# Kernel tuning notes

Hardware: AMD Instinct MI355X
Metric: run time of the kernel (lower is better)

Reference implementation:

```python
import jax, jax.numpy as jnp
import numpy as np

H = 128
G = 8192            # num session graphs
TOTAL = 409600      # total nodes across all graphs
MAX_ITEM = 10000


def setup_inputs() -> dict:
    key = jax.random.key(0)
    ks = jax.random.split(key, 16)
    rng = np.random.default_rng(0)
    # variable-length sections that sum exactly to TOTAL
    secs = rng.integers(10, 90, size=G - 1)
    last = TOTAL - int(secs.sum())
    assert last >= 1
    sections = np.concatenate([secs, [last]]).astype(np.int32)
    segment_ids = np.repeat(np.arange(G, dtype=np.int32), sections)
    last_idx = (np.cumsum(sections) - 1).astype(np.int32)

    s = 0.02
    inp = {
        "node_embedding": jax.random.normal(ks[0], (TOTAL, H), jnp.float32),
        "num_count": jax.random.uniform(ks[1], (TOTAL,), jnp.float32),
        "sections": jnp.asarray(sections),
        "segment_ids": jnp.asarray(segment_ids),
        "last_idx": jnp.asarray(last_idx),
        "item_embedding_table": jax.random.normal(ks[2], (MAX_ITEM, H), jnp.float32),
        "user_embedding": jax.random.normal(ks[3], (G, H), jnp.float32),
        "u_n_repeat": jnp.zeros((G, H), jnp.float32),
        "max_item_id": MAX_ITEM,
        "W1_w": jax.random.normal(ks[4], (H, H), jnp.float32) * s,
        "W1_b": jnp.zeros((H,), jnp.float32),
        "W2_w": jax.random.normal(ks[5], (H, H), jnp.float32) * s,
        "W2_b": jnp.zeros((H,), jnp.float32),
        "q_w": jax.random.normal(ks[6], (1, H), jnp.float32) * s,
        "q_b": jnp.zeros((1,), jnp.float32),
        "W3_w": jax.random.normal(ks[7], (H, 2 * H), jnp.float32) * s,
        "W3_b": jnp.zeros((H,), jnp.float32),
    }
    return inp


def reference(node_embedding, num_count, sections, segment_ids, last_idx,
              item_embedding_table, user_embedding, u_n_repeat, max_item_id,
              W1_w, W1_b, W2_w, W2_b, q_w, q_b, W3_w, W3_b):
    num_graphs = last_idx.shape[0]
    # last node of each graph, [G, H]
    v_n = node_embedding[last_idx]
    # broadcast last node back to every node of its graph (replaces torch.split repeat loop)
    v_n_rep = v_n[segment_ids]                          # [N, H]
    gate = jax.nn.sigmoid(v_n_rep @ W1_w.T + W1_b + node_embedding @ W2_w.T + W2_b)
    alpha = gate @ q_w.T + q_b                          # [N, 1]
    s_g_whole = num_count[:, None] * alpha * node_embedding  # [N, H]
    s_g = jax.ops.segment_sum(s_g_whole, segment_ids, num_segments=num_graphs)  # [G, H]
    s_h = jnp.concatenate([v_n, s_g], axis=1) @ W3_w.T + W3_b  # [G, H]
    return s_h
```

## Files before the change

### kernel.cpp

```cpp
#include <hip/hip_runtime.h>
#include <hip/hip_bf16.h>

#define H_DIM  128
#define NGRAPH 8192
#define NTOTAL 409600

typedef __attribute__((ext_vector_type(8))) short    s16x8;
typedef __attribute__((ext_vector_type(4))) float    f32x4;
typedef __attribute__((ext_vector_type(4))) unsigned u32x4;

__device__ __forceinline__ unsigned short f2bf(float f) {
    unsigned int u = __float_as_uint(f);
    unsigned int r = u + 0x7fffu + ((u >> 16) & 1u);
    return (unsigned short)(r >> 16);
}

__global__ void k0_w2(const float* __restrict__ W2w, unsigned short* __restrict__ w2bf) {
    int i = blockIdx.x * 256 + threadIdx.x;
    w2bf[i] = f2bf(W2w[i]);
}

__global__ __launch_bounds__(128) void k1_ag(
    const float* __restrict__ node_emb,
    const int*   __restrict__ last_idx,
    const float* __restrict__ W1w,
    const float* __restrict__ W1b,
    const float* __restrict__ W2b,
    float* __restrict__ a_g,
    float* __restrict__ s_g)
{
    __shared__ float vn[4][H_DIM];
    const int tid = threadIdx.x;
    const int g0  = blockIdx.x * 4;
    #pragma unroll
    for (int g = 0; g < 4; g++) {
        int li = last_idx[g0 + g];
        vn[g][tid] = node_emb[(size_t)li * H_DIM + tid];
        s_g[(size_t)(g0 + g) * H_DIM + tid] = 0.f;
    }
    __syncthreads();
    float b = W1b[tid] + W2b[tid];
    float a0 = b, a1 = b, a2 = b, a3 = b;
    const float* wrow = W1w + (size_t)tid * H_DIM;
    #pragma unroll 8
    for (int k = 0; k < H_DIM; k += 4) {
        float4 w = *reinterpret_cast<const float4*>(wrow + k);
        a0 += w.x * vn[0][k] + w.y * vn[0][k+1] + w.z * vn[0][k+2] + w.w * vn[0][k+3];
        a1 += w.x * vn[1][k] + w.y * vn[1][k+1] + w.z * vn[1][k+2] + w.w * vn[1][k+3];
        a2 += w.x * vn[2][k] + w.y * vn[2][k+1] + w.z * vn[2][k+2] + w.w * vn[2][k+3];
        a3 += w.x * vn[3][k] + w.y * vn[3][k+1] + w.z * vn[3][k+2] + w.w * vn[3][k+3];
    }
    a_g[(size_t)(g0 + 0) * H_DIM + tid] = a0;
    a_g[(size_t)(g0 + 1) * H_DIM + tid] = a1;
    a_g[(size_t)(g0 + 2) * H_DIM + tid] = a2;
    a_g[(size_t)(g0 + 3) * H_DIM + tid] = a3;
}

__global__ __launch_bounds__(256, 4) void k2_fused(
    const float* __restrict__ node_emb,
    const float* __restrict__ num_count,
    const int*   __restrict__ seg_ids,
    const float* __restrict__ a_g,
    const unsigned short* __restrict__ w2bf,
    const float* __restrict__ q_w,
    const float* __restrict__ q_b,
    float* __restrict__ s_g)
{
    __shared__ __align__(16) char w2s[H_DIM * 256];

    const int tid = threadIdx.x;
    {
        const uint4* wsrc = reinterpret_cast<const uint4*>(w2bf);
        #pragma unroll
        for (int i = 0; i < 8; i++) {
            int c = i * 256 + tid;
            uint4 v = wsrc[c];
            int byte = c << 4;
            int row  = byte >> 8;
            *reinterpret_cast<uint4*>(w2s + (byte ^ ((row & 7) << 4))) = v;
        }
    }

    const int lane = tid & 63;
    const int wid  = tid >> 6;
    const int l16 = lane & 15, lq = lane >> 4;
    const int nb  = (blockIdx.x * 4 + wid) * 16;

    const int   sgl = seg_ids[nb + l16];
    const float ncl = num_count[nb + l16];
    const float qb0 = q_b[0];

    s16x8 af[4];
    const float* nrow = node_emb + (size_t)(nb + l16) * H_DIM + lq * 8;
    #pragma unroll
    for (int ks = 0; ks < 4; ks++) {
        float4 f0 = *reinterpret_cast<const float4*>(nrow + ks * 32);
        float4 f1 = *reinterpret_cast<const float4*>(nrow + ks * 32 + 4);
        unsigned p0, p1, p2, p3;
        asm("v_cvt_pk_bf16_f32 %0, %1, %2" : "=v"(p0) : "v"(f0.x), "v"(f0.y));
        asm("v_cvt_pk_bf16_f32 %0, %1, %2" : "=v"(p1) : "v"(f0.z), "v"(f0.w));
        asm("v_cvt_pk_bf16_f32 %0, %1, %2" : "=v"(p2) : "v"(f1.x), "v"(f1.y));
        asm("v_cvt_pk_bf16_f32 %0, %1, %2" : "=v"(p3) : "v"(f1.z), "v"(f1.w));
        union { u32x4 u; s16x8 s; } cv;
        cv.u = u32x4{p0, p1, p2, p3};
        af[ks] = cv.s;
    }

    __syncthreads();

    f32x4 acc[8];
    #pragma unroll
    for (int nt = 0; nt < 8; nt++) acc[nt] = f32x4{0.f, 0.f, 0.f, 0.f};
    #pragma unroll
    for (int ks = 0; ks < 4; ks++) {
        #pragma unroll
        for (int nt = 0; nt < 8; nt++) {
            int row  = nt * 16 + l16;
            int byte = (row << 8) | ((lq * 8 + ks * 32) << 1);
            byte ^= (row & 7) << 4;
            s16x8 wfr = *reinterpret_cast<const s16x8*>(w2s + byte);
            acc[nt] = __builtin_amdgcn_mfma_f32_16x16x32_bf16(wfr, af[ks], acc[nt], 0, 0, 0);
        }
    }
    __builtin_amdgcn_sched_barrier(0);

    const float* agrow = a_g + (size_t)sgl * H_DIM + lq * 4;
    float p = 0.f;
    #pragma unroll
    for (int nt = 0; nt < 8; nt++) {
        float4 q4 = *reinterpret_cast<const float4*>(q_w + nt * 16 + lq * 4);
        float4 a4 = *reinterpret_cast<const float4*>(agrow + nt * 16);
        float zq[4] = {a4.x, a4.y, a4.z, a4.w};
        float qq[4] = {q4.x, q4.y, q4.z, q4.w};
        #pragma unroll
        for (int rr = 0; rr < 4; rr++) {
            float z = acc[nt][rr] + zq[rr];
            float e = __expf(-z);
            p += qq[rr] * __builtin_amdgcn_rcpf(1.f + e);
        }
    }
    p += __shfl_xor(p, 16, 64);
    p += __shfl_xor(p, 32, 64);
    const float coefl = ncl * (p + qb0);

    s16x8 ib[2];
    #pragma unroll
    for (int b = 0; b < 2; b++) {
        int kk = l16 + 16 * b;
        #pragma unroll
        for (int e = 0; e < 8; e++)
            ib[b][e] = (kk == lq * 8 + e) ? (short)0x3F80 : (short)0;
    }
    f32x4 accT[4][2];
    #pragma unroll
    for (int ks = 0; ks < 4; ks++)
        #pragma unroll
        for (int b = 0; b < 2; b++)
            accT[ks][b] = __builtin_amdgcn_mfma_f32_16x16x32_bf16(
                              af[ks], ib[b], f32x4{0.f, 0.f, 0.f, 0.f}, 0, 0, 0);

    int r0 = 0;
    while (r0 < 16) {
        const int cur = __shfl(sgl, r0, 64);
        unsigned long long diff = __ballot(sgl != cur) & 0xFFFFull;
        diff &= ~((1ull << r0) - 1ull);
        const int r1 = diff ? (int)__builtin_ctzll(diff) : 16;

        const float cmask = (sgl == cur) ? coefl : 0.f;
        float cm[4];
        #pragma unroll
        for (int rr = 0; rr < 4; rr++)
            cm[rr] = __shfl(cmask, lq * 4 + rr, 64);

        #pragma unroll
        for (int ks = 0; ks < 4; ks++) {
            #pragma unroll
            for (int b = 0; b < 2; b++) {
                float s = cm[0] * accT[ks][b][0] + cm[1] * accT[ks][b][1]
                        + cm[2] * accT[ks][b][2] + cm[3] * accT[ks][b][3];
                s += __shfl_xor(s, 16, 64);
                s += __shfl_xor(s, 32, 64);
                if (lq == 0)
                    atomicAdd(s_g + (size_t)cur * H_DIM + ks * 32 + b * 16 + l16, s);
            }
        }
        r0 = r1;
    }
}

__global__ __launch_bounds__(128) void k3_out(
    const float* __restrict__ node_emb,
    const int*   __restrict__ last_idx,
    const float* __restrict__ s_g,
    const float* __restrict__ W3w,
    const float* __restrict__ W3b,
    float* __restrict__ out)
{
    __shared__ float cat[8][2 * H_DIM];
    const int tid = threadIdx.x;
    const int g0  = blockIdx.x * 8;
    #pragma unroll
    for (int g = 0; g < 8; g++) {
        cat[g][tid]         = node_emb[(size_t)last_idx[g0 + g] * H_DIM + tid];
        cat[g][H_DIM + tid] = s_g[(size_t)(g0 + g) * H_DIM + tid];
    }
    __syncthreads();
    float acc[8];
    float b = W3b[tid];
    #pragma unroll
    for (int g = 0; g < 8; g++) acc[g] = b;
    const float* wrow = W3w + (size_t)tid * (2 * H_DIM);
    for (int k = 0; k < 2 * H_DIM; k += 4) {
        float4 w = *reinterpret_cast<const float4*>(wrow + k);
        #pragma unroll
        for (int g = 0; g < 8; g++)
            acc[g] += w.x * cat[g][k] + w.y * cat[g][k+1]
                    + w.z * cat[g][k+2] + w.w * cat[g][k+3];
    }
    #pragma unroll
    for (int g = 0; g < 8; g++)
        out[(size_t)(g0 + g) * H_DIM + tid] = acc[g];
}

extern "C" void kernel_launch(void* const* d_in, const int* in_sizes, int n_in,
                              void* d_out, int out_size, void* d_ws, size_t ws_size,
                              hipStream_t stream) {
    const float* node_emb  = (const float*)d_in[0];
    const float* num_count = (const float*)d_in[1];
    const int*   seg_ids   = (const int*)d_in[3];
    const int*   last_idx  = (const int*)d_in[4];
    const float* W1w = (const float*)d_in[9];
    const float* W1b = (const float*)d_in[10];
    const float* W2w = (const float*)d_in[11];
    const float* W2b = (const float*)d_in[12];
    const float* qw  = (const float*)d_in[13];
    const float* qb  = (const float*)d_in[14];
    const float* W3w = (const float*)d_in[15];
    const float* W3b = (const float*)d_in[16];
    float* out = (float*)d_out;

    char* ws = (char*)d_ws;
    float* a_g = (float*)(ws);
    float* s_g = (float*)(ws + (4u << 20));
    unsigned short* w2bf = (unsigned short*)(ws + (8u << 20));

    k0_w2   <<<64,          256, 0, stream>>>(W2w, w2bf);
    k1_ag   <<<NGRAPH / 4,  128, 0, stream>>>(node_emb, last_idx, W1w, W1b, W2b, a_g, s_g);
    k2_fused<<<NTOTAL / 64, 256, 0, stream>>>(node_emb, num_count, seg_ids, a_g,
                                              w2bf, qw, qb, s_g);
    k3_out  <<<NGRAPH / 8,  128, 0, stream>>>(node_emb, last_idx, s_g, W3w, W3b, out);
}
```

Before: 109.1 us.

## Make k2 waves loop over four node tiles with register prefetch

Each wave in the fused gate/segment-sum kernel now handles four 16-node tiles in a loop instead of one. The next tile's node rows, segment ids and counts are loaded into registers while the current tile is computed. The W2 LDS staging cost is spread over four times as many nodes, and the gate GEMM is split into two halves to limit accumulator registers. The grid shrinks by four and the occupancy hint drops from 4 to 3 blocks per CU, so there is less parallelism to hide latency.

```diff
diff --git a/kernel.cpp b/kernel.cpp
--- a/kernel.cpp
+++ b/kernel.cpp
@@ -56,7 +56,7 @@
     a_g[(size_t)(g0 + 3) * H_DIM + tid] = a3;
 }
 
-__global__ __launch_bounds__(256, 4) void k2_fused(
+__global__ __launch_bounds__(256, 3) void k2_fused(
     const float* __restrict__ node_emb,
     const float* __restrict__ num_count,
     const int*   __restrict__ seg_ids,
@@ -84,64 +84,8 @@
     const int lane = tid & 63;
     const int wid  = tid >> 6;
     const int l16 = lane & 15, lq = lane >> 4;
-    const int nb  = (blockIdx.x * 4 + wid) * 16;
-
-    const int   sgl = seg_ids[nb + l16];
-    const float ncl = num_count[nb + l16];
+    const int nbw = (blockIdx.x * 4 + wid) * 64;
     const float qb0 = q_b[0];
-
-    s16x8 af[4];
-    const float* nrow = node_emb + (size_t)(nb + l16) * H_DIM + lq * 8;
-    #pragma unroll
-    for (int ks = 0; ks < 4; ks++) {
-        float4 f0 = *reinterpret_cast<const float4*>(nrow + ks * 32);
-        float4 f1 = *reinterpret_cast<const float4*>(nrow + ks * 32 + 4);
-        unsigned p0, p1, p2, p3;
-        asm("v_cvt_pk_bf16_f32 %0, %1, %2" : "=v"(p0) : "v"(f0.x), "v"(f0.y));
-        asm("v_cvt_pk_bf16_f32 %0, %1, %2" : "=v"(p1) : "v"(f0.z), "v"(f0.w));
-        asm("v_cvt_pk_bf16_f32 %0, %1, %2" : "=v"(p2) : "v"(f1.x), "v"(f1.y));
-        asm("v_cvt_pk_bf16_f32 %0, %1, %2" : "=v"(p3) : "v"(f1.z), "v"(f1.w));
-        union { u32x4 u; s16x8 s; } cv;
-        cv.u = u32x4{p0, p1, p2, p3};
-        af[ks] = cv.s;
-    }
-
-    __syncthreads();
-
-    f32x4 acc[8];
-    #pragma unroll
-    for (int nt = 0; nt < 8; nt++) acc[nt] = f32x4{0.f, 0.f, 0.f, 0.f};
-    #pragma unroll
-    for (int ks = 0; ks < 4; ks++) {
-        #pragma unroll
-        for (int nt = 0; nt < 8; nt++) {
-            int row  = nt * 16 + l16;
-            int byte = (row << 8) | ((lq * 8 + ks * 32) << 1);
-            byte ^= (row & 7) << 4;
-            s16x8 wfr = *reinterpret_cast<const s16x8*>(w2s + byte);
-            acc[nt] = __builtin_amdgcn_mfma_f32_16x16x32_bf16(wfr, af[ks], acc[nt], 0, 0, 0);
-        }
-    }
-    __builtin_amdgcn_sched_barrier(0);
-
-    const float* agrow = a_g + (size_t)sgl * H_DIM + lq * 4;
-    float p = 0.f;
-    #pragma unroll
-    for (int nt = 0; nt < 8; nt++) {
-        float4 q4 = *reinterpret_cast<const float4*>(q_w + nt * 16 + lq * 4);
-        float4 a4 = *reinterpret_cast<const float4*>(agrow + nt * 16);
-        float zq[4] = {a4.x, a4.y, a4.z, a4.w};
-        float qq[4] = {q4.x, q4.y, q4.z, q4.w};
-        #pragma unroll
-        for (int rr = 0; rr < 4; rr++) {
-            float z = acc[nt][rr] + zq[rr];
-            float e = __expf(-z);
-            p += qq[rr] * __builtin_amdgcn_rcpf(1.f + e);
-        }
-    }
-    p += __shfl_xor(p, 16, 64);
-    p += __shfl_xor(p, 32, 64);
-    const float coefl = ncl * (p + qb0);
 
     s16x8 ib[2];
     #pragma unroll
@@ -151,40 +95,153 @@
         for (int e = 0; e < 8; e++)
             ib[b][e] = (kk == lq * 8 + e) ? (short)0x3F80 : (short)0;
     }
-    f32x4 accT[4][2];
-    #pragma unroll
-    for (int ks = 0; ks < 4; ks++)
-        #pragma unroll
-        for (int b = 0; b < 2; b++)
-            accT[ks][b] = __builtin_amdgcn_mfma_f32_16x16x32_bf16(
-                              af[ks], ib[b], f32x4{0.f, 0.f, 0.f, 0.f}, 0, 0, 0);
-
-    int r0 = 0;
-    while (r0 < 16) {
-        const int cur = __shfl(sgl, r0, 64);
-        unsigned long long diff = __ballot(sgl != cur) & 0xFFFFull;
-        diff &= ~((1ull << r0) - 1ull);
-        const int r1 = diff ? (int)__builtin_ctzll(diff) : 16;
-
-        const float cmask = (sgl == cur) ? coefl : 0.f;
-        float cm[4];
-        #pragma unroll
-        for (int rr = 0; rr < 4; rr++)
-            cm[rr] = __shfl(cmask, lq * 4 + rr, 64);
-
+
+    float4 rA[8];
+    int   sgN;
+    float ncN;
+    {
+        const float* nrow = node_emb + (size_t)(nbw + l16) * H_DIM + lq * 8;
         #pragma unroll
         for (int ks = 0; ks < 4; ks++) {
-            #pragma unroll
-            for (int b = 0; b < 2; b++) {
-                float s = cm[0] * accT[ks][b][0] + cm[1] * accT[ks][b][1]
-                        + cm[2] * accT[ks][b][2] + cm[3] * accT[ks][b][3];
-                s += __shfl_xor(s, 16, 64);
-                s += __shfl_xor(s, 32, 64);
-                if (lq == 0)
-                    atomicAdd(s_g + (size_t)cur * H_DIM + ks * 32 + b * 16 + l16, s);
-            }
-        }
-        r0 = r1;
+            rA[2 * ks]     = *reinterpret_cast<const float4*>(nrow + ks * 32);
+            rA[2 * ks + 1] = *reinterpret_cast<const float4*>(nrow + ks * 32 + 4);
+        }
+        sgN = seg_ids[nbw + l16];
+        ncN = num_count[nbw + l16];
+    }
+
+    __syncthreads();
+
+    #pragma unroll 1
+    for (int t = 0; t < 4; t++) {
+        const int   nb  = nbw + t * 16;
+        const int   sgl = sgN;
+        const float ncl = ncN;
+
+        s16x8 af[4];
+        #pragma unroll
+        for (int ks = 0; ks < 4; ks++) {
+            unsigned p0, p1, p2, p3;
+            asm("v_cvt_pk_bf16_f32 %0, %1, %2" : "=v"(p0) : "v"(rA[2*ks].x),   "v"(rA[2*ks].y));
+            asm("v_cvt_pk_bf16_f32 %0, %1, %2" : "=v"(p1) : "v"(rA[2*ks].z),   "v"(rA[2*ks].w));
+            asm("v_cvt_pk_bf16_f32 %0, %1, %2" : "=v"(p2) : "v"(rA[2*ks+1].x), "v"(rA[2*ks+1].y));
+            asm("v_cvt_pk_bf16_f32 %0, %1, %2" : "=v"(p3) : "v"(rA[2*ks+1].z), "v"(rA[2*ks+1].w));
+            union { u32x4 u; s16x8 s; } cv;
+            cv.u = u32x4{p0, p1, p2, p3};
+            af[ks] = cv.s;
+        }
+
+        if (t < 3) {
+            const float* nrow = node_emb + (size_t)(nb + 16 + l16) * H_DIM + lq * 8;
+            #pragma unroll
+            for (int ks = 0; ks < 4; ks++) {
+                rA[2 * ks]     = *reinterpret_cast<const float4*>(nrow + ks * 32);
+                rA[2 * ks + 1] = *reinterpret_cast<const float4*>(nrow + ks * 32 + 4);
+            }
+            sgN = seg_ids[nb + 16 + l16];
+            ncN = num_count[nb + 16 + l16];
+        }
+        __builtin_amdgcn_sched_barrier(0);
+
+        float p = 0.f;
+        const float* agrow = a_g + (size_t)sgl * H_DIM + lq * 4;
+        {
+            f32x4 accA[4];
+            #pragma unroll
+            for (int nt = 0; nt < 4; nt++) accA[nt] = f32x4{0.f, 0.f, 0.f, 0.f};
+            #pragma unroll
+            for (int ks = 0; ks < 4; ks++) {
+                #pragma unroll
+                for (int nt = 0; nt < 4; nt++) {
+                    int row  = nt * 16 + l16;
+                    int byte = (row << 8) | ((lq * 8 + ks * 32) << 1);
+                    byte ^= (row & 7) << 4;
+                    s16x8 wfr = *reinterpret_cast<const s16x8*>(w2s + byte);
+                    accA[nt] = __builtin_amdgcn_mfma_f32_16x16x32_bf16(wfr, af[ks], accA[nt], 0, 0, 0);
+                }
+            }
+            #pragma unroll
+            for (int nt = 0; nt < 4; nt++) {
+                float4 q4 = *reinterpret_cast<const float4*>(q_w + nt * 16 + lq * 4);
+                float4 a4 = *reinterpret_cast<const float4*>(agrow + nt * 16);
+                float zq[4] = {a4.x, a4.y, a4.z, a4.w};
+                float qq[4] = {q4.x, q4.y, q4.z, q4.w};
+                #pragma unroll
+                for (int rr = 0; rr < 4; rr++) {
+                    float z = accA[nt][rr] + zq[rr];
+                    float e = __expf(-z);
+                    p += qq[rr] * __builtin_amdgcn_rcpf(1.f + e);
+                }
+            }
+        }
+        {
+            f32x4 accB[4];
+            #pragma unroll
+            for (int nt = 0; nt < 4; nt++) accB[nt] = f32x4{0.f, 0.f, 0.f, 0.f};
+            #pragma unroll
+            for (int ks = 0; ks < 4; ks++) {
+                #pragma unroll
+                for (int nt = 0; nt < 4; nt++) {
+                    int row  = (nt + 4) * 16 + l16;
+                    int byte = (row << 8) | ((lq * 8 + ks * 32) << 1);
+                    byte ^= (row & 7) << 4;
+                    s16x8 wfr = *reinterpret_cast<const s16x8*>(w2s + byte);
+                    accB[nt] = __builtin_amdgcn_mfma_f32_16x16x32_bf16(wfr, af[ks], accB[nt], 0, 0, 0);
+                }
+            }
+            #pragma unroll
+            for (int nt = 0; nt < 4; nt++) {
+                float4 q4 = *reinterpret_cast<const float4*>(q_w + (nt + 4) * 16 + lq * 4);
+                float4 a4 = *reinterpret_cast<const float4*>(agrow + (nt + 4) * 16);
+                float zq[4] = {a4.x, a4.y, a4.z, a4.w};
+                float qq[4] = {q4.x, q4.y, q4.z, q4.w};
+                #pragma unroll
+                for (int rr = 0; rr < 4; rr++) {
+                    float z = accB[nt][rr] + zq[rr];
+                    float e = __expf(-z);
+                    p += qq[rr] * __builtin_amdgcn_rcpf(1.f + e);
+                }
+            }
+        }
+        p += __shfl_xor(p, 16, 64);
+        p += __shfl_xor(p, 32, 64);
+        const float coefl = ncl * (p + qb0);
+
+        f32x4 accT[4][2];
+        #pragma unroll
+        for (int ks = 0; ks < 4; ks++)
+            #pragma unroll
+            for (int b = 0; b < 2; b++)
+                accT[ks][b] = __builtin_amdgcn_mfma_f32_16x16x32_bf16(
+                                  af[ks], ib[b], f32x4{0.f, 0.f, 0.f, 0.f}, 0, 0, 0);
+
+        int r0 = 0;
+        while (r0 < 16) {
+            const int cur = __shfl(sgl, r0, 64);
+            unsigned long long diff = __ballot(sgl != cur) & 0xFFFFull;
+            diff &= ~((1ull << r0) - 1ull);
+            const int r1 = diff ? (int)__builtin_ctzll(diff) : 16;
+
+            const float cmask = (sgl == cur) ? coefl : 0.f;
+            float cm[4];
+            #pragma unroll
+            for (int rr = 0; rr < 4; rr++)
+                cm[rr] = __shfl(cmask, lq * 4 + rr, 64);
+
+            #pragma unroll
+            for (int ks = 0; ks < 4; ks++) {
+                #pragma unroll
+                for (int b = 0; b < 2; b++) {
+                    float s = cm[0] * accT[ks][b][0] + cm[1] * accT[ks][b][1]
+                            + cm[2] * accT[ks][b][2] + cm[3] * accT[ks][b][3];
+                    s += __shfl_xor(s, 16, 64);
+                    s += __shfl_xor(s, 32, 64);
+                    if (lq == 0)
+                        atomicAdd(s_g + (size_t)cur * H_DIM + ks * 32 + b * 16 + l16, s);
+                }
+            }
+            r0 = r1;
+        }
     }
 }
 
@@ -244,9 +301,9 @@
     float* s_g = (float*)(ws + (4u << 20));
     unsigned short* w2bf = (unsigned short*)(ws + (8u << 20));
 
-    k0_w2   <<<64,          256, 0, stream>>>(W2w, w2bf);
-    k1_ag   <<<NGRAPH / 4,  128, 0, stream>>>(node_emb, last_idx, W1w, W1b, W2b, a_g, s_g);
-    k2_fused<<<NTOTAL / 64, 256, 0, stream>>>(node_emb, num_count, seg_ids, a_g,
-                                              w2bf, qw, qb, s_g);
-    k3_out  <<<NGRAPH / 8,  128, 0, stream>>>(node_emb, last_idx, s_g, W3w, W3b, out);
-}
+    k0_w2   <<<64,           256, 0, stream>>>(W2w, w2bf);
+    k1_ag   <<<NGRAPH / 4,   128, 0, stream>>>(node_emb, last_idx, W1w, W1b, W2b, a_g, s_g);
+    k2_fused<<<NTOTAL / 256, 256, 0, stream>>>(node_emb, num_count, seg_ids, a_g,
+                                               w2bf, qw, qb, s_g);
+    k3_out  <<<NGRAPH / 8,   128, 0, stream>>>(node_emb, last_idx, s_g, W3w, W3b, out);
+}
```

Result: no change. 109.8 us (+0.6%).

## Assign one wave per graph segment and accumulate segment sums in registers

Applied to the files above, without the earlier changes.

The fused gate/segment-sum kernel now maps each wavefront to one whole graph, walking its nodes in 16-row chunks and accumulating the segment sum in registers. A single direct store per output row replaces the per-chunk atomicAdds. The oversized last graph is split across extra tail waves that still use atomics. This removes the per-chunk segment-boundary ballot loops and most global atomics, but adds load imbalance from variable graph lengths and wasted lanes on partial chunks.

```diff
diff --git a/kernel.cpp b/kernel.cpp
--- a/kernel.cpp
+++ b/kernel.cpp
@@ -4,6 +4,7 @@
 #define H_DIM  128
 #define NGRAPH 8192
 #define NTOTAL 409600
+#define TAILW  512
 
 typedef __attribute__((ext_vector_type(8))) short    s16x8;
 typedef __attribute__((ext_vector_type(4))) float    f32x4;
@@ -59,7 +60,7 @@
 __global__ __launch_bounds__(256, 4) void k2_fused(
     const float* __restrict__ node_emb,
     const float* __restrict__ num_count,
-    const int*   __restrict__ seg_ids,
+    const int*   __restrict__ last_idx,
     const float* __restrict__ a_g,
     const unsigned short* __restrict__ w2bf,
     const float* __restrict__ q_w,
@@ -82,66 +83,27 @@
     }
 
     const int lane = tid & 63;
-    const int wid  = tid >> 6;
     const int l16 = lane & 15, lq = lane >> 4;
-    const int nb  = (blockIdx.x * 4 + wid) * 16;
-
-    const int   sgl = seg_ids[nb + l16];
-    const float ncl = num_count[nb + l16];
-    const float qb0 = q_b[0];
-
-    s16x8 af[4];
-    const float* nrow = node_emb + (size_t)(nb + l16) * H_DIM + lq * 8;
-    #pragma unroll
-    for (int ks = 0; ks < 4; ks++) {
-        float4 f0 = *reinterpret_cast<const float4*>(nrow + ks * 32);
-        float4 f1 = *reinterpret_cast<const float4*>(nrow + ks * 32 + 4);
-        unsigned p0, p1, p2, p3;
-        asm("v_cvt_pk_bf16_f32 %0, %1, %2" : "=v"(p0) : "v"(f0.x), "v"(f0.y));
-        asm("v_cvt_pk_bf16_f32 %0, %1, %2" : "=v"(p1) : "v"(f0.z), "v"(f0.w));
-        asm("v_cvt_pk_bf16_f32 %0, %1, %2" : "=v"(p2) : "v"(f1.x), "v"(f1.y));
-        asm("v_cvt_pk_bf16_f32 %0, %1, %2" : "=v"(p3) : "v"(f1.z), "v"(f1.w));
-        union { u32x4 u; s16x8 s; } cv;
-        cv.u = u32x4{p0, p1, p2, p3};
-        af[ks] = cv.s;
-    }
-
-    __syncthreads();
-
-    f32x4 acc[8];
-    #pragma unroll
-    for (int nt = 0; nt < 8; nt++) acc[nt] = f32x4{0.f, 0.f, 0.f, 0.f};
-    #pragma unroll
-    for (int ks = 0; ks < 4; ks++) {
-        #pragma unroll
-        for (int nt = 0; nt < 8; nt++) {
-            int row  = nt * 16 + l16;
-            int byte = (row << 8) | ((lq * 8 + ks * 32) << 1);
-            byte ^= (row & 7) << 4;
-            s16x8 wfr = *reinterpret_cast<const s16x8*>(w2s + byte);
-            acc[nt] = __builtin_amdgcn_mfma_f32_16x16x32_bf16(wfr, af[ks], acc[nt], 0, 0, 0);
-        }
-    }
-    __builtin_amdgcn_sched_barrier(0);
-
-    const float* agrow = a_g + (size_t)sgl * H_DIM + lq * 4;
-    float p = 0.f;
-    #pragma unroll
-    for (int nt = 0; nt < 8; nt++) {
-        float4 q4 = *reinterpret_cast<const float4*>(q_w + nt * 16 + lq * 4);
-        float4 a4 = *reinterpret_cast<const float4*>(agrow + nt * 16);
-        float zq[4] = {a4.x, a4.y, a4.z, a4.w};
-        float qq[4] = {q4.x, q4.y, q4.z, q4.w};
-        #pragma unroll
-        for (int rr = 0; rr < 4; rr++) {
-            float z = acc[nt][rr] + zq[rr];
-            float e = __expf(-z);
-            p += qq[rr] * __builtin_amdgcn_rcpf(1.f + e);
-        }
-    }
-    p += __shfl_xor(p, 16, 64);
-    p += __shfl_xor(p, 32, 64);
-    const float coefl = ncl * (p + qb0);
+    const int item = __builtin_amdgcn_readfirstlane(blockIdx.x * 4 + (tid >> 6));
+
+    int g = 0, nstart = 0, nend = -1;
+    bool tail = false, valid = true;
+    if (item < NGRAPH - 1) {
+        g      = item;
+        nstart = item ? (last_idx[item - 1] + 1) : 0;
+        nend   = last_idx[item];
+    } else if (item < NGRAPH - 1 + TAILW) {
+        g    = NGRAPH - 1;
+        tail = true;
+        int base = last_idx[NGRAPH - 2] + 1;
+        int t0   = item - (NGRAPH - 1);
+        nstart   = base + t0 * 16;
+        int ge   = last_idx[NGRAPH - 1];
+        if (nstart > ge) valid = false;
+        else nend = min(ge, nstart + 15);
+    } else {
+        valid = false;
+    }
 
     s16x8 ib[2];
     #pragma unroll
@@ -151,40 +113,112 @@
         for (int e = 0; e < 8; e++)
             ib[b][e] = (kk == lq * 8 + e) ? (short)0x3F80 : (short)0;
     }
-    f32x4 accT[4][2];
-    #pragma unroll
-    for (int ks = 0; ks < 4; ks++)
-        #pragma unroll
-        for (int b = 0; b < 2; b++)
-            accT[ks][b] = __builtin_amdgcn_mfma_f32_16x16x32_bf16(
-                              af[ks], ib[b], f32x4{0.f, 0.f, 0.f, 0.f}, 0, 0, 0);
-
-    int r0 = 0;
-    while (r0 < 16) {
-        const int cur = __shfl(sgl, r0, 64);
-        unsigned long long diff = __ballot(sgl != cur) & 0xFFFFull;
-        diff &= ~((1ull << r0) - 1ull);
-        const int r1 = diff ? (int)__builtin_ctzll(diff) : 16;
-
-        const float cmask = (sgl == cur) ? coefl : 0.f;
-        float cm[4];
-        #pragma unroll
-        for (int rr = 0; rr < 4; rr++)
-            cm[rr] = __shfl(cmask, lq * 4 + rr, 64);
-
+
+    __syncthreads();
+    if (!valid) return;
+
+    const float qb0 = q_b[0];
+    const float* agrow = a_g + (size_t)g * H_DIM;
+
+    float sgacc[4][2] = {{0.f, 0.f}, {0.f, 0.f}, {0.f, 0.f}, {0.f, 0.f}};
+
+    for (int nb = nstart; nb <= nend; nb += 16) {
+        const int vcnt = nend - nb + 1;
+        const int idx  = min(nb + l16, nend);
+
+        const float* nrow = node_emb + (size_t)idx * H_DIM + lq * 8;
+        float4 f[8];
+        #pragma unroll
+        for (int ks = 0; ks < 4; ks++) {
+            f[2 * ks]     = *reinterpret_cast<const float4*>(nrow + ks * 32);
+            f[2 * ks + 1] = *reinterpret_cast<const float4*>(nrow + ks * 32 + 4);
+        }
+        const float ncl = num_count[idx];
+
+        s16x8 af[4];
+        #pragma unroll
+        for (int ks = 0; ks < 4; ks++) {
+            unsigned p0, p1, p2, p3;
+            asm("v_cvt_pk_bf16_f32 %0, %1, %2" : "=v"(p0) : "v"(f[2*ks].x),   "v"(f[2*ks].y));
+            asm("v_cvt_pk_bf16_f32 %0, %1, %2" : "=v"(p1) : "v"(f[2*ks].z),   "v"(f[2*ks].w));
+            asm("v_cvt_pk_bf16_f32 %0, %1, %2" : "=v"(p2) : "v"(f[2*ks+1].x), "v"(f[2*ks+1].y));
+            asm("v_cvt_pk_bf16_f32 %0, %1, %2" : "=v"(p3) : "v"(f[2*ks+1].z), "v"(f[2*ks+1].w));
+            union { u32x4 u; s16x8 s; } cv;
+            cv.u = u32x4{p0, p1, p2, p3};
+            af[ks] = cv.s;
+        }
+
+        f32x4 accT[4][2];
+        #pragma unroll
+        for (int ks = 0; ks < 4; ks++)
+            #pragma unroll
+            for (int b = 0; b < 2; b++)
+                accT[ks][b] = __builtin_amdgcn_mfma_f32_16x16x32_bf16(
+                                  af[ks], ib[b], f32x4{0.f, 0.f, 0.f, 0.f}, 0, 0, 0);
+
+        f32x4 acc[8];
+        #pragma unroll
+        for (int nt = 0; nt < 8; nt++) acc[nt] = f32x4{0.f, 0.f, 0.f, 0.f};
         #pragma unroll
         for (int ks = 0; ks < 4; ks++) {
             #pragma unroll
-            for (int b = 0; b < 2; b++) {
-                float s = cm[0] * accT[ks][b][0] + cm[1] * accT[ks][b][1]
-                        + cm[2] * accT[ks][b][2] + cm[3] * accT[ks][b][3];
-                s += __shfl_xor(s, 16, 64);
-                s += __shfl_xor(s, 32, 64);
-                if (lq == 0)
-                    atomicAdd(s_g + (size_t)cur * H_DIM + ks * 32 + b * 16 + l16, s);
+            for (int nt = 0; nt < 8; nt++) {
+                int row  = nt * 16 + l16;
+                int byte = (row << 8) | ((lq * 8 + ks * 32) << 1);
+                byte ^= (row & 7) << 4;
+                s16x8 wfr = *reinterpret_cast<const s16x8*>(w2s + byte);
+                acc[nt] = __builtin_amdgcn_mfma_f32_16x16x32_bf16(wfr, af[ks], acc[nt], 0, 0, 0);
             }
         }
-        r0 = r1;
+
+        float pp0 = 0.f, pp1 = 0.f, pp2 = 0.f, pp3 = 0.f;
+        #pragma unroll
+        for (int nt = 0; nt < 8; nt++) {
+            float4 q4 = *reinterpret_cast<const float4*>(q_w + nt * 16 + lq * 4);
+            float4 a4 = *reinterpret_cast<const float4*>(agrow + nt * 16 + lq * 4);
+            float z0 = acc[nt][0] + a4.x;
+            float z1 = acc[nt][1] + a4.y;
+            float z2 = acc[nt][2] + a4.z;
+            float z3 = acc[nt][3] + a4.w;
+            pp0 += q4.x * __builtin_amdgcn_rcpf(1.f + __expf(-z0));
+            pp1 += q4.y * __builtin_amdgcn_rcpf(1.f + __expf(-z1));
+            pp2 += q4.z * __builtin_amdgcn_rcpf(1.f + __expf(-z2));
+            pp3 += q4.w * __builtin_amdgcn_rcpf(1.f + __expf(-z3));
+        }
+        float p = (pp0 + pp1) + (pp2 + pp3);
+        p += __shfl_xor(p, 16, 64);
+        p += __shfl_xor(p, 32, 64);
+        const float coefl = ncl * (p + qb0);
+
+        float cm[4];
+        #pragma unroll
+        for (int rr = 0; rr < 4; rr++) {
+            int r = lq * 4 + rr;
+            float c = __shfl(coefl, r, 64);
+            cm[rr] = (r < vcnt) ? c : 0.f;
+        }
+
+        #pragma unroll
+        for (int ks = 0; ks < 4; ks++)
+            #pragma unroll
+            for (int b = 0; b < 2; b++)
+                sgacc[ks][b] += cm[0] * accT[ks][b][0] + cm[1] * accT[ks][b][1]
+                              + cm[2] * accT[ks][b][2] + cm[3] * accT[ks][b][3];
+    }
+
+    #pragma unroll
+    for (int ks = 0; ks < 4; ks++) {
+        #pragma unroll
+        for (int b = 0; b < 2; b++) {
+            float s = sgacc[ks][b];
+            s += __shfl_xor(s, 16, 64);
+            s += __shfl_xor(s, 32, 64);
+            if (lq == 0) {
+                float* dst = s_g + (size_t)g * H_DIM + ks * 32 + b * 16 + l16;
+                if (tail) atomicAdd(dst, s);
+                else      *dst = s;
+            }
+        }
     }
 }
 
@@ -227,7 +261,6 @@
                               hipStream_t stream) {
     const float* node_emb  = (const float*)d_in[0];
     const float* num_count = (const float*)d_in[1];
-    const int*   seg_ids   = (const int*)d_in[3];
     const int*   last_idx  = (const int*)d_in[4];
     const float* W1w = (const float*)d_in[9];
     const float* W1b = (const float*)d_in[10];
@@ -244,9 +277,12 @@
     float* s_g = (float*)(ws + (4u << 20));
     unsigned short* w2bf = (unsigned short*)(ws + (8u << 20));
 
-    k0_w2   <<<64,          256, 0, stream>>>(W2w, w2bf);
-    k1_ag   <<<NGRAPH / 4,  128, 0, stream>>>(node_emb, last_idx, W1w, W1b, W2b, a_g, s_g);
-    k2_fused<<<NTOTAL / 64, 256, 0, stream>>>(node_emb, num_count, seg_ids, a_g,
-                                              w2bf, qw, qb, s_g);
-    k3_out  <<<NGRAPH / 8,  128, 0, stream>>>(node_emb, last_idx, s_g, W3w, W3b, out);
-}
+    const int items  = (NGRAPH - 1) + TAILW;
+    const int blocks = (items + 3) / 4;
+
+    k0_w2   <<<64,         256, 0, stream>>>(W2w, w2bf);
+    k1_ag   <<<NGRAPH / 4, 128, 0, stream>>>(node_emb, last_idx, W1w, W1b, W2b, a_g, s_g);
+    k2_fused<<<blocks,     256, 0, stream>>>(node_emb, num_count, last_idx, a_g,
+                                             w2bf, qw, qb, s_g);
+    k3_out  <<<NGRAPH / 8, 128, 0, stream>>>(node_emb, last_idx, s_g, W3w, W3b, out);
+}
```

Result: slower. 129.6 us (+18.7%).

## Read W2 fragments directly from global memory instead of staging in LDS

Applied to the files above, without the earlier changes.

Removes the per-block copy of the bf16 W2 matrix into swizzled shared memory and the barrier that followed it. MFMA weight fragments are now loaded straight from global memory, relying on L1/L2 caching because every block reads the same 32KB. Freeing the LDS raises the occupancy hint to 6 blocks per CU, and the sigmoid/q reduction is split into four independent accumulators for more ILP. The risk is higher global/L1 traffic and latency on the MFMA inner loop, plus register pressure from the tighter launch bound.

```diff
diff --git a/kernel.cpp b/kernel.cpp
--- a/kernel.cpp
+++ b/kernel.cpp
@@ -56,7 +56,7 @@
     a_g[(size_t)(g0 + 3) * H_DIM + tid] = a3;
 }
 
-__global__ __launch_bounds__(256, 4) void k2_fused(
+__global__ __launch_bounds__(256, 6) void k2_fused(
     const float* __restrict__ node_emb,
     const float* __restrict__ num_count,
     const int*   __restrict__ seg_ids,
@@ -66,25 +66,10 @@
     const float* __restrict__ q_b,
     float* __restrict__ s_g)
 {
-    __shared__ __align__(16) char w2s[H_DIM * 256];
-
-    const int tid = threadIdx.x;
-    {
-        const uint4* wsrc = reinterpret_cast<const uint4*>(w2bf);
-        #pragma unroll
-        for (int i = 0; i < 8; i++) {
-            int c = i * 256 + tid;
-            uint4 v = wsrc[c];
-            int byte = c << 4;
-            int row  = byte >> 8;
-            *reinterpret_cast<uint4*>(w2s + (byte ^ ((row & 7) << 4))) = v;
-        }
-    }
-
+    const int tid  = threadIdx.x;
     const int lane = tid & 63;
-    const int wid  = tid >> 6;
     const int l16 = lane & 15, lq = lane >> 4;
-    const int nb  = (blockIdx.x * 4 + wid) * 16;
+    const int nb  = (blockIdx.x * 4 + (tid >> 6)) * 16;
 
     const int   sgl = seg_ids[nb + l16];
     const float ncl = num_count[nb + l16];
@@ -106,8 +91,6 @@
         af[ks] = cv.s;
     }
 
-    __syncthreads();
-
     f32x4 acc[8];
     #pragma unroll
     for (int nt = 0; nt < 8; nt++) acc[nt] = f32x4{0.f, 0.f, 0.f, 0.f};
@@ -115,30 +98,28 @@
     for (int ks = 0; ks < 4; ks++) {
         #pragma unroll
         for (int nt = 0; nt < 8; nt++) {
-            int row  = nt * 16 + l16;
-            int byte = (row << 8) | ((lq * 8 + ks * 32) << 1);
-            byte ^= (row & 7) << 4;
-            s16x8 wfr = *reinterpret_cast<const s16x8*>(w2s + byte);
+            s16x8 wfr = *reinterpret_cast<const s16x8*>(
+                w2bf + (size_t)(nt * 16 + l16) * H_DIM + lq * 8 + ks * 32);
             acc[nt] = __builtin_amdgcn_mfma_f32_16x16x32_bf16(wfr, af[ks], acc[nt], 0, 0, 0);
         }
     }
-    __builtin_amdgcn_sched_barrier(0);
 
     const float* agrow = a_g + (size_t)sgl * H_DIM + lq * 4;
-    float p = 0.f;
+    float pp0 = 0.f, pp1 = 0.f, pp2 = 0.f, pp3 = 0.f;
     #pragma unroll
     for (int nt = 0; nt < 8; nt++) {
         float4 q4 = *reinterpret_cast<const float4*>(q_w + nt * 16 + lq * 4);
         float4 a4 = *reinterpret_cast<const float4*>(agrow + nt * 16);
-        float zq[4] = {a4.x, a4.y, a4.z, a4.w};
-        float qq[4] = {q4.x, q4.y, q4.z, q4.w};
-        #pragma unroll
-        for (int rr = 0; rr < 4; rr++) {
-            float z = acc[nt][rr] + zq[rr];
-            float e = __expf(-z);
-            p += qq[rr] * __builtin_amdgcn_rcpf(1.f + e);
-        }
-    }
+        float z0 = acc[nt][0] + a4.x;
+        float z1 = acc[nt][1] + a4.y;
+        float z2 = acc[nt][2] + a4.z;
+        float z3 = acc[nt][3] + a4.w;
+        pp0 += q4.x * __builtin_amdgcn_rcpf(1.f + __expf(-z0));
+        pp1 += q4.y * __builtin_amdgcn_rcpf(1.f + __expf(-z1));
+        pp2 += q4.z * __builtin_amdgcn_rcpf(1.f + __expf(-z2));
+        pp3 += q4.w * __builtin_amdgcn_rcpf(1.f + __expf(-z3));
+    }
+    float p = (pp0 + pp1) + (pp2 + pp3);
     p += __shfl_xor(p, 16, 64);
     p += __shfl_xor(p, 32, 64);
     const float coefl = ncl * (p + qb0);
```

Measured after the change: 189.3 us. 73.4% more time.
